# Kernel optimization log

Hardware: AMD Instinct MI355X
Metric: run time of the kernel (lower is better)

The kernel has to match this reference:

```python
import jax, jax.numpy as jnp
import numpy as np

N = 50000   # nodes
E = 800000  # edges (avg degree 16)
D = 256     # hidden_dims
V = 3       # num_views
C = 10      # num_classes


def setup_inputs() -> dict:
    key = jax.random.key(0)
    ks = jax.random.split(key, 24)
    def nrm(k, shp, scale):
        return jax.random.normal(k, shp, dtype=jnp.float32) * jnp.float32(scale)
    dims = [1000, 800, 600]
    inp = {}
    for i, d in enumerate(dims):
        inp[f"x{i}"] = nrm(ks[i], (N, d), 1.0)
        inp[f"p{i}w1"] = nrm(ks[3 + 2 * i], (d, D), 1.0 / np.sqrt(d))
        inp[f"p{i}w2"] = nrm(ks[4 + 2 * i], (D, D), 1.0 / np.sqrt(D))
    inp["edge_row"] = jax.random.randint(ks[10], (E,), 0, N)
    inp["edge_col"] = jax.random.randint(ks[11], (E,), 0, N)
    inp["edge_val"] = jax.random.uniform(ks[12], (E,), dtype=jnp.float32) / 16.0  # ~normalized adj values
    inp["vw1"] = nrm(ks[13], (V, 1), 1.0)
    inp["vw2"] = nrm(ks[14], (1, V), 1.0)
    inp["fw1"] = nrm(ks[15], (D, 16), 1.0 / np.sqrt(D))
    inp["fw2"] = nrm(ks[16], (16, D), 0.25)
    inp["m1"] = nrm(ks[17], (D + V, D // 2), 1.0 / np.sqrt(D + V))
    inp["m2"] = nrm(ks[18], (D // 2, D + V), 1.0 / np.sqrt(D // 2))
    inp["g0"] = nrm(ks[19], (D + V, D + V), 1.0 / np.sqrt(D + V))
    inp["g1"] = nrm(ks[20], (D + V, D + V), 1.0 / np.sqrt(D + V))
    inp["g2"] = nrm(ks[21], (D + V, C), 1.0 / np.sqrt(D + V))
    return inp


def _spmm(row, col, val, x):
    # torch.spmm(adj, x) with adj given as COO edge list
    return jax.ops.segment_sum(val[:, None] * x[col], row, num_segments=N)


def reference(x0, x1, x2, p0w1, p0w2, p1w1, p1w2, p2w1, p2w2,
              edge_row, edge_col, edge_val,
              vw1, vw2, fw1, fw2, m1, m2, g0, g1, g2):
    # per-view projection MLPs (bias-free, dropout off in eval)
    h0 = jax.nn.relu(x0 @ p0w1) @ p0w2
    h1 = jax.nn.relu(x1 @ p1w1) @ p1w2
    h2 = jax.nn.relu(x2 @ p2w1) @ p2w2
    h = jnp.stack([h0, h1, h2], axis=2)  # [N, D, V]

    pool_view = h.mean(axis=1)  # [N, V]
    pool_feat = h.mean(axis=2)  # [N, D]
    view_x = jax.nn.sigmoid(jax.nn.relu(pool_view @ vw1) @ vw2)  # [N, V]
    feat_x = jax.nn.sigmoid(jax.nn.relu(pool_feat @ fw1) @ fw2)  # [N, D]

    vf = jax.nn.relu(jnp.concatenate([view_x, feat_x], axis=1) @ m1) @ m2  # [N, V+D]
    view_w = jax.nn.sigmoid(vf[:, :V])[:, None, :]  # [N, 1, V]
    feat_w = jax.nn.sigmoid(vf[:, V:])[:, :, None]  # [N, D, 1]

    out1 = h * view_w
    out2 = h * feat_w
    # fus_type == 'self': [N, V] ++ [N, D] -> [N, D+V]
    z = jnp.concatenate([out1.mean(axis=1), out2.mean(axis=2)], axis=1)

    # 3-layer GCN: spmm -> linear -> tanh (tanh also on last layer per default activation)
    for g in (g0, g1, g2):
        z = jnp.tanh(_spmm(edge_row, edge_col, edge_val, z) @ g)
    return z
```

## Files before the change

### kernel.cpp

```cpp
#include <hip/hip_runtime.h>
#include <hip/hip_bf16.h>
#include <cmath>
#include <cstdint>

using bf16 = __bf16;
typedef __bf16 bf16x8 __attribute__((ext_vector_type(8)));
typedef __bf16 bf16x4 __attribute__((ext_vector_type(4)));
typedef float f32x4 __attribute__((ext_vector_type(4)));

#define DEVI __device__ __forceinline__

DEVI int pcidx(int m, int c) { return (m << 2) + (c ^ ((m >> 1) & 3)); }

DEVI void gload16(const void* g, void* l) {
  __builtin_amdgcn_global_load_lds(
      (const __attribute__((address_space(1))) void*)g,
      (__attribute__((address_space(3))) void*)l, 16, 0, 0);
}

template <int ACT, bool AF32>
__global__ __launch_bounds__(256) void gemm_k(
    const void* __restrict__ Ap, const bf16* __restrict__ Bt,
    void* __restrict__ Cp, int Mreal, int K, int ldA, int Ncols, int ldC,
    float scale, int NT, const float* __restrict__ pfx,
    const float* __restrict__ pvx) {
  __shared__ __align__(16) bf16 lA[128 * 32];
  __shared__ __align__(16) bf16 lB[128 * 32];
  const int tid = threadIdx.x;
  const int nwg = gridDim.x;
  const int q8 = nwg >> 3, r8 = nwg & 7;
  const int xcd = blockIdx.x & 7, idx = blockIdx.x >> 3;
  const int wgid =
      (xcd < r8 ? xcd * (q8 + 1) : r8 * (q8 + 1) + (xcd - r8) * q8) + idx;
  const int m0 = (wgid / NT) * 128, n0 = (wgid % NT) * 128;

  const int w = tid >> 6, lane = tid & 63;
  const int wm = w >> 1, wn = w & 1;
  const int lm = lane & 15, lg = lane >> 4;

  f32x4 acc[4][4] = {};

  const int nkt = K / 32;
  for (int kt = 0; kt < nkt; ++kt) {
    const int k0 = kt * 32;
#pragma unroll
    for (int i = 0; i < 2; i++) {
      int q = i * 256 + tid;
      int row = q >> 2, slot = q & 3;
      int c = slot ^ ((row >> 1) & 3);
      const bf16* src = Bt + (size_t)(n0 + row) * K + k0 + c * 8;
      bf16* dst = lB + (size_t)(i * 256 + (tid & 192)) * 8;
      gload16(src, dst);
    }
    if constexpr (AF32) {
      const float* Af = (const float*)Ap;
      int row = tid >> 1, h = tid & 1;
      int gm = m0 + row;
      int kb = k0 + h * 16;
      const float* Ar = Af + (size_t)gm * ldA;
      bf16x8 v0, v1;
      if (gm < Mreal && kb + 16 <= ldA) {
        f32x4 f0 = *(const f32x4*)(Ar + kb);
        f32x4 f1 = *(const f32x4*)(Ar + kb + 4);
        f32x4 f2 = *(const f32x4*)(Ar + kb + 8);
        f32x4 f3 = *(const f32x4*)(Ar + kb + 12);
#pragma unroll
        for (int j = 0; j < 4; j++) {
          v0[j] = (bf16)f0[j];
          v0[4 + j] = (bf16)f1[j];
          v1[j] = (bf16)f2[j];
          v1[4 + j] = (bf16)f3[j];
        }
      } else {
#pragma unroll
        for (int j = 0; j < 8; j++) {
          v0[j] = (bf16)((gm < Mreal && kb + j < ldA) ? Ar[kb + j] : 0.f);
          v1[j] = (bf16)((gm < Mreal && kb + 8 + j < ldA) ? Ar[kb + 8 + j] : 0.f);
        }
      }
      *(bf16x8*)&lA[(size_t)pcidx(row, h * 2) * 8] = v0;
      *(bf16x8*)&lA[(size_t)pcidx(row, h * 2 + 1) * 8] = v1;
    } else {
      const bf16* Ab = (const bf16*)Ap;
#pragma unroll
      for (int i = 0; i < 2; i++) {
        int q = i * 256 + tid;
        int row = q >> 2, slot = q & 3;
        int c = slot ^ ((row >> 1) & 3);
        const bf16* src = Ab + (size_t)(m0 + row) * K + k0 + c * 8;
        bf16* dst = lA + (size_t)(i * 256 + (tid & 192)) * 8;
        gload16(src, dst);
      }
    }
    asm volatile("s_waitcnt vmcnt(0)" ::: "memory");
    __syncthreads();
    bf16x8 af[4], bfr[4];
#pragma unroll
    for (int mi = 0; mi < 4; ++mi) {
      int m = wm * 64 + mi * 16 + lm;
      af[mi] = *(const bf16x8*)&lA[(size_t)pcidx(m, lg) * 8];
    }
#pragma unroll
    for (int ni = 0; ni < 4; ++ni) {
      int n = wn * 64 + ni * 16 + lm;
      bfr[ni] = *(const bf16x8*)&lB[(size_t)pcidx(n, lg) * 8];
    }
#pragma unroll
    for (int mi = 0; mi < 4; ++mi)
#pragma unroll
      for (int ni = 0; ni < 4; ++ni)
        acc[mi][ni] = __builtin_amdgcn_mfma_f32_16x16x32_bf16(
            af[mi], bfr[ni], acc[mi][ni], 0, 0, 0);
    __syncthreads();
  }
#pragma unroll
  for (int mi = 0; mi < 4; ++mi) {
#pragma unroll
    for (int ni = 0; ni < 4; ++ni) {
#pragma unroll
      for (int r = 0; r < 4; ++r) {
        int row = m0 + wm * 64 + mi * 16 + lg * 4 + r;
        int col = n0 + wn * 64 + ni * 16 + lm;
        if (row < Mreal && col < Ncols) {
          float x = acc[mi][ni][r] * scale;
          if constexpr (ACT == 0)
            ((float*)Cp)[(size_t)row * ldC + col] = x;
          else if constexpr (ACT == 1)
            ((bf16*)Cp)[(size_t)row * ldC + col] = (bf16)fmaxf(x, 0.f);
          else if constexpr (ACT == 3)
            ((bf16*)Cp)[(size_t)row * ldC + col] = (bf16)tanhf(x);
          else if constexpr (ACT == 4)
            ((float*)Cp)[(size_t)row * ldC + col] = tanhf(x);
          else if constexpr (ACT == 5) {
            float sig = 1.f / (1.f + __expf(-x));
            float mul;
            if (col >= 32) mul = pfx[(size_t)row * 256 + (col - 32)];
            else if (col < 3) mul = pvx[(size_t)row * 4 + col];
            else mul = 0.f;
            ((bf16*)Cp)[(size_t)row * ldC + col] = (bf16)(sig * mul);
          }
        }
      }
    }
  }
}

struct WJob {
  const float* src;
  bf16* dst;
  int Np, W, K, Nsrc, sN, Kp, cofs, kch, blkEnd;
};
struct WJobs { WJob j[14]; };

__global__ void wcvt_k(WJobs J) {
  int b = blockIdx.x;
  int ji = 0;
  while (b >= J.j[ji].blkEnd) ji++;
  const WJob job = J.j[ji];
  int lb = b - (ji ? J.j[ji - 1].blkEnd : 0);
  int n = lb / job.kch, bk = lb % job.kch;
  int k = bk * 256 + (int)threadIdx.x;
  if (k >= job.W) return;
  float v = 0.f;
  if (k < job.K && n < job.Nsrc) v = job.src[(size_t)k * job.sN + n];
  job.dst[(size_t)n * job.Kp + job.cofs + k] = (bf16)v;
}

__global__ void w2rs_k(const float* w0, const float* w1, const float* w2,
                       float* out) {
  int v = blockIdx.x, k = threadIdx.x;
  const float* w = v == 0 ? w0 : (v == 1 ? w1 : w2);
  float s = 0.f;
  for (int d = 0; d < 256; d++) s += w[(size_t)k * 256 + d];
  out[v * 256 + k] = s;
}

__global__ __launch_bounds__(256) void gate_k(
    const bf16* __restrict__ t, const float* __restrict__ pf,
    const float* __restrict__ w2rs, const float* __restrict__ vw1,
    const float* __restrict__ vw2, const float* __restrict__ fw1,
    const float* __restrict__ fw2, bf16* __restrict__ c,
    float* __restrict__ pv, int N) {
  __shared__ __align__(16) float pfs[4][260];
  __shared__ __align__(16) float usm[4][16];
  const int wid = threadIdx.x >> 6, lane = threadIdx.x & 63;
  const int n = blockIdx.x * 4 + wid;
  if (n >= N) return;
  const int g = lane >> 4, j = lane & 15;

  f32x4 pfv = *(const f32x4*)(pf + (size_t)n * 256 + lane * 4);
  *(f32x4*)&pfs[wid][lane * 4] = pfv;

  size_t tb = (size_t)n * 768;
  bf16x4 t0 = *(const bf16x4*)(t + tb + lane * 4);
  bf16x4 t1 = *(const bf16x4*)(t + tb + 256 + lane * 4);
  bf16x4 t2 = *(const bf16x4*)(t + tb + 512 + lane * 4);
  f32x4 wr0 = *(const f32x4*)(w2rs + lane * 4);
  f32x4 wr1 = *(const f32x4*)(w2rs + 256 + lane * 4);
  f32x4 wr2 = *(const f32x4*)(w2rs + 512 + lane * 4);
  float s0 = 0.f, s1 = 0.f, s2 = 0.f;
#pragma unroll
  for (int cc = 0; cc < 4; cc++) {
    s0 += (float)t0[cc] * wr0[cc];
    s1 += (float)t1[cc] * wr1[cc];
    s2 += (float)t2[cc] * wr2[cc];
  }
#pragma unroll
  for (int o = 32; o > 0; o >>= 1) {
    s0 += __shfl_xor(s0, o);
    s1 += __shfl_xor(s1, o);
    s2 += __shfl_xor(s2, o);
  }
  const float p0 = s0 * (1.f / 256.f), p1 = s1 * (1.f / 256.f),
              p2 = s2 * (1.f / 256.f);
  const float av = fmaxf(p0 * vw1[0] + p1 * vw1[1] + p2 * vw1[2], 0.f);
  const float vx0 = 1.f / (1.f + __expf(-av * vw2[0]));
  const float vx1 = 1.f / (1.f + __expf(-av * vw2[1]));
  const float vx2 = 1.f / (1.f + __expf(-av * vw2[2]));

  __builtin_amdgcn_wave_barrier();
  float uj = 0.f;
#pragma unroll
  for (int kk = 0; kk < 64; kk++) {
    int k = g * 64 + ((kk + g * 8) & 63);
    uj += pfs[wid][k] * fw1[k * 16 + j];
  }
  uj += __shfl_xor(uj, 16);
  uj += __shfl_xor(uj, 32);
  uj = fmaxf(uj, 0.f);
  if (lane < 16) usm[wid][lane] = uj;
  __builtin_amdgcn_wave_barrier();

  float ur[16];
  *(f32x4*)&ur[0] = *(const f32x4*)&usm[wid][0];
  *(f32x4*)&ur[4] = *(const f32x4*)&usm[wid][4];
  *(f32x4*)&ur[8] = *(const f32x4*)&usm[wid][8];
  *(f32x4*)&ur[12] = *(const f32x4*)&usm[wid][12];
  f32x4 fx = {0.f, 0.f, 0.f, 0.f};
#pragma unroll
  for (int jj = 0; jj < 16; jj++) {
    f32x4 wv = *(const f32x4*)(fw2 + (size_t)jj * 256 + lane * 4);
#pragma unroll
    for (int cc = 0; cc < 4; cc++) fx[cc] += ur[jj] * wv[cc];
  }
  size_t cb = (size_t)n * 288;
  bf16x4 outv;
#pragma unroll
  for (int cc = 0; cc < 4; cc++)
    outv[cc] = (bf16)(1.f / (1.f + __expf(-fx[cc])));
  *(bf16x4*)(c + cb + 32 + lane * 4) = outv;
  if (lane < 8) {
    bf16x4 hv;
#pragma unroll
    for (int cc = 0; cc < 4; cc++) {
      int pos = lane * 4 + cc;
      float vv = pos == 0 ? vx0 : (pos == 1 ? vx1 : (pos == 2 ? vx2 : 0.f));
      hv[cc] = (bf16)vv;
    }
    *(bf16x4*)(c + cb + lane * 4) = hv;
  }
  if (lane < 3) pv[(size_t)n * 4 + lane] = lane == 0 ? p0 : (lane == 1 ? p1 : p2);
}

__global__ void zero_k(int* p, int n) {
  int i = blockIdx.x * 256 + threadIdx.x;
  if (i < n) p[i] = 0;
}
__global__ void hist_k(const int* __restrict__ row, int* __restrict__ cnt, int E) {
  int e = blockIdx.x * 256 + threadIdx.x;
  if (e < E) atomicAdd(&cnt[row[e]], 1);
}
__global__ void s1_k(const int* cnt, int* bsum, int n) {
  __shared__ int sh[256];
  int i = blockIdx.x * 256 + threadIdx.x;
  sh[threadIdx.x] = (i < n) ? cnt[i] : 0;
  __syncthreads();
  for (int o = 128; o > 0; o >>= 1) {
    if ((int)threadIdx.x < o) sh[threadIdx.x] += sh[threadIdx.x + o];
    __syncthreads();
  }
  if (threadIdx.x == 0) bsum[blockIdx.x] = sh[0];
}
__global__ void s2_k(const int* bsum, int* bofs, int nb) {
  __shared__ int sh[256];
  int t = threadIdx.x;
  int v = (t < nb) ? bsum[t] : 0;
  sh[t] = v;
  __syncthreads();
  for (int o = 1; o < 256; o <<= 1) {
    int add = (t >= o) ? sh[t - o] : 0;
    __syncthreads();
    sh[t] += add;
    __syncthreads();
  }
  if (t < nb) bofs[t] = sh[t] - v;
}
__global__ void s3_k(const int* cnt, const int* bofs, int* starts, int* cursor,
                     int n, int total) {
  __shared__ int sh[256];
  int t = threadIdx.x, i = blockIdx.x * 256 + t;
  int v = (i < n) ? cnt[i] : 0;
  sh[t] = v;
  __syncthreads();
  for (int o = 1; o < 256; o <<= 1) {
    int add = (t >= o) ? sh[t - o] : 0;
    __syncthreads();
    sh[t] += add;
    __syncthreads();
  }
  if (i < n) {
    int ex = bofs[blockIdx.x] + sh[t] - v;
    starts[i] = ex;
    cursor[i] = ex;
  }
  if (i == 0) starts[n] = total;
}
__global__ void scat_k(const int* __restrict__ row, const int* __restrict__ col,
                       const float* __restrict__ val, int* __restrict__ cursor,
                       int* __restrict__ ccol, float* __restrict__ cval, int E) {
  int e = blockIdx.x * 256 + threadIdx.x;
  if (e < E) {
    int r = row[e];
    int p = atomicAdd(&cursor[r], 1);
    ccol[p] = col[e];
    cval[p] = val[e];
  }
}

__global__ __launch_bounds__(256) void spmm_k(
    const int* __restrict__ starts, const int* __restrict__ ccol,
    const float* __restrict__ cval, const bf16* __restrict__ z,
    bf16* __restrict__ s) {
  int r = blockIdx.x, t = threadIdx.x;
  int e0 = starts[r], e1 = starts[r + 1];
  float a0 = 0.f, a1 = 0.f;
  int e = e0;
  for (; e + 4 <= e1; e += 4) {
    int c0 = ccol[e], c1 = ccol[e + 1], c2 = ccol[e + 2], c3 = ccol[e + 3];
    float v0 = cval[e], v1 = cval[e + 1], v2 = cval[e + 2], v3 = cval[e + 3];
    const bf16* z0 = z + (size_t)c0 * 288;
    const bf16* z1 = z + (size_t)c1 * 288;
    const bf16* z2 = z + (size_t)c2 * 288;
    const bf16* z3 = z + (size_t)c3 * 288;
    float b0 = (float)z0[t], b1 = (float)z1[t], b2 = (float)z2[t],
          b3 = (float)z3[t];
    a0 += v0 * b0 + v1 * b1 + v2 * b2 + v3 * b3;
    if (t < 32) {
      a1 += v0 * (float)z0[256 + t] + v1 * (float)z1[256 + t] +
            v2 * (float)z2[256 + t] + v3 * (float)z3[256 + t];
    }
  }
  for (; e < e1; e++) {
    int cc = ccol[e];
    float v = cval[e];
    const bf16* zp = z + (size_t)cc * 288;
    a0 += v * (float)zp[t];
    if (t < 32) a1 += v * (float)zp[256 + t];
  }
  size_t sb = (size_t)r * 288;
  s[sb + t] = (bf16)a0;
  if (t < 32) s[sb + 256 + t] = (bf16)a1;
}

extern "C" void kernel_launch(void* const* d_in, const int* in_sizes, int n_in,
                              void* d_out, int out_size, void* d_ws,
                              size_t ws_size, hipStream_t stream) {
  const float* x0 = (const float*)d_in[0];
  const float* p0w1 = (const float*)d_in[1];
  const float* p0w2 = (const float*)d_in[2];
  const float* x1 = (const float*)d_in[3];
  const float* p1w1 = (const float*)d_in[4];
  const float* p1w2 = (const float*)d_in[5];
  const float* x2 = (const float*)d_in[6];
  const float* p2w1 = (const float*)d_in[7];
  const float* p2w2 = (const float*)d_in[8];
  const int* erow = (const int*)d_in[9];
  const int* ecol = (const int*)d_in[10];
  const float* evalp = (const float*)d_in[11];
  const float* vw1 = (const float*)d_in[12];
  const float* vw2 = (const float*)d_in[13];
  const float* fw1 = (const float*)d_in[14];
  const float* fw2 = (const float*)d_in[15];
  const float* m1 = (const float*)d_in[16];
  const float* m2 = (const float*)d_in[17];
  const float* g0 = (const float*)d_in[18];
  const float* g1 = (const float*)d_in[19];
  const float* g2 = (const float*)d_in[20];

  const int N = 50000;
  const int MP = 50048;
  const int NB = 391;
  const int E = in_sizes[9];

  char* p = (char*)d_ws;
  auto alloc = [&](size_t bytes) -> char* {
    char* r = p;
    p += (bytes + 255) & ~(size_t)255;
    return r;
  };
  bf16* t = (bf16*)alloc((size_t)MP * 768 * 2);
  bf16* w1T0 = (bf16*)alloc((size_t)256 * 1024 * 2);
  bf16* w1T1 = (bf16*)alloc((size_t)256 * 832 * 2);
  bf16* w1T2 = (bf16*)alloc((size_t)256 * 640 * 2);
  bf16* W2sT = (bf16*)alloc((size_t)256 * 768 * 2);
  float* w2rs = (float*)alloc(768 * 4);
  bf16* m1T = (bf16*)alloc((size_t)128 * 288 * 2);
  bf16* m2T = (bf16*)alloc((size_t)384 * 128 * 2);
  bf16* g0T = (bf16*)alloc((size_t)384 * 288 * 2);
  bf16* g1T = (bf16*)alloc((size_t)384 * 288 * 2);
  bf16* g2T = (bf16*)alloc((size_t)128 * 288 * 2);
  float* pf = (float*)alloc((size_t)N * 256 * 4);
  float* pv = (float*)alloc((size_t)N * 4 * 4);
  bf16* c = (bf16*)alloc((size_t)MP * 288 * 2);
  int* cnt = (int*)alloc((size_t)50004 * 4);
  int* starts = (int*)alloc((size_t)50004 * 4);
  int* cursor = (int*)alloc((size_t)50004 * 4);
  int* bsum = (int*)alloc(1024);
  int* bofs = (int*)alloc(1024);
  int* ccol = (int*)alloc((size_t)E * 4);
  float* cval = (float*)alloc((size_t)E * 4);
  bf16* u = t;
  bf16* z = t + (size_t)MP * 416;
  bf16* s = c;
  if ((size_t)(p - (char*)d_ws) > ws_size) return;

  WJobs J;
  auto setj = [&](int idx, const float* src, bf16* dst, int Np, int W, int K,
                  int Nsrc, int sN, int Kp, int cofs) {
    WJob& jj = J.j[idx];
    jj.src = src; jj.dst = dst; jj.Np = Np; jj.W = W; jj.K = K; jj.Nsrc = Nsrc;
    jj.sN = sN; jj.Kp = Kp; jj.cofs = cofs; jj.kch = (W + 255) / 256;
    jj.blkEnd = 0;
  };
  setj(0, p0w1, w1T0, 256, 1024, 1000, 256, 256, 1024, 0);
  setj(1, p1w1, w1T1, 256, 832, 800, 256, 256, 832, 0);
  setj(2, p2w1, w1T2, 256, 640, 600, 256, 256, 640, 0);
  setj(3, p0w2, W2sT, 256, 256, 256, 256, 256, 768, 0);
  setj(4, p1w2, W2sT, 256, 256, 256, 256, 256, 768, 256);
  setj(5, p2w2, W2sT, 256, 256, 256, 256, 256, 768, 512);
  setj(6, m1, m1T, 128, 32, 3, 128, 128, 288, 0);
  setj(7, m1 + 3 * 128, m1T, 128, 256, 256, 128, 128, 288, 32);
  setj(8, m2, m2T, 32, 128, 128, 3, 259, 128, 0);
  setj(9, m2 + 3, m2T + (size_t)32 * 128, 256, 128, 128, 256, 259, 128, 0);
  setj(10, g0, g0T, 384, 32, 3, 259, 259, 288, 0);
  setj(11, g0 + 3 * 259, g0T, 384, 256, 256, 259, 259, 288, 32);
  setj(12, g1, g1T, 384, 288, 259, 259, 259, 288, 0);
  setj(13, g2, g2T, 128, 288, 259, 10, 10, 288, 0);
  int cum = 0;
  for (int i = 0; i < 14; i++) {
    cum += J.j[i].Np * J.j[i].kch;
    J.j[i].blkEnd = cum;
  }
  wcvt_k<<<cum, 256, 0, stream>>>(J);
  w2rs_k<<<3, 256, 0, stream>>>(p0w2, p1w2, p2w2, w2rs);

  gemm_k<1, true><<<NB * 2, 256, 0, stream>>>(x0, w1T0, t, N, 1024, 1000, 256, 768, 1.f, 2, nullptr, nullptr);
  gemm_k<1, true><<<NB * 2, 256, 0, stream>>>(x1, w1T1, t + 256, N, 832, 800, 256, 768, 1.f, 2, nullptr, nullptr);
  gemm_k<1, true><<<NB * 2, 256, 0, stream>>>(x2, w1T2, t + 512, N, 640, 600, 256, 768, 1.f, 2, nullptr, nullptr);
  gemm_k<0, false><<<NB * 2, 256, 0, stream>>>(t, W2sT, pf, N, 768, 768, 256, 256, 1.f / 3.f, 2, nullptr, nullptr);
  gate_k<<<(N + 3) / 4, 256, 0, stream>>>(t, pf, w2rs, vw1, vw2, fw1, fw2, c, pv, N);
  gemm_k<1, false><<<NB * 1, 256, 0, stream>>>(c, m1T, u, N, 288, 288, 128, 128, 1.f, 1, nullptr, nullptr);
  gemm_k<5, false><<<NB * 3, 256, 0, stream>>>(u, m2T, z, N, 128, 128, 288, 288, 1.f, 3, pf, pv);

  zero_k<<<196, 256, 0, stream>>>(cnt, N);
  hist_k<<<(E + 255) / 256, 256, 0, stream>>>(erow, cnt, E);
  s1_k<<<196, 256, 0, stream>>>(cnt, bsum, N);
  s2_k<<<1, 256, 0, stream>>>(bsum, bofs, 196);
  s3_k<<<196, 256, 0, stream>>>(cnt, bofs, starts, cursor, N, E);
  scat_k<<<(E + 255) / 256, 256, 0, stream>>>(erow, ecol, evalp, cursor, ccol, cval, E);

  spmm_k<<<N, 256, 0, stream>>>(starts, ccol, cval, z, s);
  gemm_k<3, false><<<NB * 3, 256, 0, stream>>>(s, g0T, z, N, 288, 288, 288, 288, 1.f, 3, nullptr, nullptr);
  spmm_k<<<N, 256, 0, stream>>>(starts, ccol, cval, z, s);
  gemm_k<3, false><<<NB * 3, 256, 0, stream>>>(s, g1T, z, N, 288, 288, 288, 288, 1.f, 3, nullptr, nullptr);
  spmm_k<<<N, 256, 0, stream>>>(starts, ccol, cval, z, s);
  gemm_k<4, false><<<NB * 1, 256, 0, stream>>>(s, g2T, d_out, N, 288, 288, 10, 10, 1.f, 1, nullptr, nullptr);
}
```

Baseline: 1.278 ms.

## Double-buffer GEMM LDS tiles and merge three view projection GEMMs into one launch

Gives the bf16 GEMM two LDS buffers so the next K-tile's global-to-LDS loads are issued before the MFMAs on the current tile, and drops the per-iteration trailing barrier. Adds a separate gemm3_k that runs all three fp32-input first-layer projections in a single launch through a job table. That kernel prefetches the next fp32 A tile into registers during compute and converts it to bf16 afterwards. The intent is to hide memory latency behind MFMA work and cut launch and tail overhead, at the cost of twice the LDS per block and more registers, which may lower occupancy.

```diff
diff --git a/kernel.cpp b/kernel.cpp
--- a/kernel.cpp
+++ b/kernel.cpp
@@ -18,20 +18,21 @@
       (__attribute__((address_space(3))) void*)l, 16, 0, 0);
 }
 
-template <int ACT, bool AF32>
+DEVI int xcd_swz(int lb, int nwg) {
+  int q8 = nwg >> 3, r8 = nwg & 7;
+  int xcd = lb & 7, idx = lb >> 3;
+  return (xcd < r8 ? xcd * (q8 + 1) : r8 * (q8 + 1) + (xcd - r8) * q8) + idx;
+}
+
+template <int ACT>
 __global__ __launch_bounds__(256) void gemm_k(
-    const void* __restrict__ Ap, const bf16* __restrict__ Bt,
-    void* __restrict__ Cp, int Mreal, int K, int ldA, int Ncols, int ldC,
-    float scale, int NT, const float* __restrict__ pfx,
-    const float* __restrict__ pvx) {
-  __shared__ __align__(16) bf16 lA[128 * 32];
-  __shared__ __align__(16) bf16 lB[128 * 32];
+    const bf16* __restrict__ Ab, const bf16* __restrict__ Bt,
+    void* __restrict__ Cp, int Mreal, int K, int Ncols, int ldC, float scale,
+    int NT, const float* __restrict__ pfx, const float* __restrict__ pvx) {
+  __shared__ __align__(16) bf16 lA[2][128 * 32];
+  __shared__ __align__(16) bf16 lB[2][128 * 32];
   const int tid = threadIdx.x;
-  const int nwg = gridDim.x;
-  const int q8 = nwg >> 3, r8 = nwg & 7;
-  const int xcd = blockIdx.x & 7, idx = blockIdx.x >> 3;
-  const int wgid =
-      (xcd < r8 ? xcd * (q8 + 1) : r8 * (q8 + 1) + (xcd - r8) * q8) + idx;
+  const int wgid = xcd_swz(blockIdx.x, gridDim.x);
   const int m0 = (wgid / NT) * 128, n0 = (wgid % NT) * 128;
 
   const int w = tid >> 6, lane = tid & 63;
@@ -40,70 +41,41 @@
 
   f32x4 acc[4][4] = {};
 
-  const int nkt = K / 32;
-  for (int kt = 0; kt < nkt; ++kt) {
-    const int k0 = kt * 32;
+  auto issueAB = [&](int buf, int k0) {
 #pragma unroll
     for (int i = 0; i < 2; i++) {
       int q = i * 256 + tid;
       int row = q >> 2, slot = q & 3;
       int c = slot ^ ((row >> 1) & 3);
-      const bf16* src = Bt + (size_t)(n0 + row) * K + k0 + c * 8;
-      bf16* dst = lB + (size_t)(i * 256 + (tid & 192)) * 8;
-      gload16(src, dst);
-    }
-    if constexpr (AF32) {
-      const float* Af = (const float*)Ap;
-      int row = tid >> 1, h = tid & 1;
-      int gm = m0 + row;
-      int kb = k0 + h * 16;
-      const float* Ar = Af + (size_t)gm * ldA;
-      bf16x8 v0, v1;
-      if (gm < Mreal && kb + 16 <= ldA) {
-        f32x4 f0 = *(const f32x4*)(Ar + kb);
-        f32x4 f1 = *(const f32x4*)(Ar + kb + 4);
-        f32x4 f2 = *(const f32x4*)(Ar + kb + 8);
-        f32x4 f3 = *(const f32x4*)(Ar + kb + 12);
-#pragma unroll
-        for (int j = 0; j < 4; j++) {
-          v0[j] = (bf16)f0[j];
-          v0[4 + j] = (bf16)f1[j];
-          v1[j] = (bf16)f2[j];
-          v1[4 + j] = (bf16)f3[j];
-        }
-      } else {
-#pragma unroll
-        for (int j = 0; j < 8; j++) {
-          v0[j] = (bf16)((gm < Mreal && kb + j < ldA) ? Ar[kb + j] : 0.f);
-          v1[j] = (bf16)((gm < Mreal && kb + 8 + j < ldA) ? Ar[kb + 8 + j] : 0.f);
-        }
-      }
-      *(bf16x8*)&lA[(size_t)pcidx(row, h * 2) * 8] = v0;
-      *(bf16x8*)&lA[(size_t)pcidx(row, h * 2 + 1) * 8] = v1;
-    } else {
-      const bf16* Ab = (const bf16*)Ap;
-#pragma unroll
-      for (int i = 0; i < 2; i++) {
-        int q = i * 256 + tid;
-        int row = q >> 2, slot = q & 3;
-        int c = slot ^ ((row >> 1) & 3);
-        const bf16* src = Ab + (size_t)(m0 + row) * K + k0 + c * 8;
-        bf16* dst = lA + (size_t)(i * 256 + (tid & 192)) * 8;
-        gload16(src, dst);
-      }
-    }
-    asm volatile("s_waitcnt vmcnt(0)" ::: "memory");
-    __syncthreads();
+      gload16(Bt + (size_t)(n0 + row) * K + k0 + c * 8,
+              &lB[buf][(size_t)(i * 256 + (tid & 192)) * 8]);
+    }
+#pragma unroll
+    for (int i = 0; i < 2; i++) {
+      int q = i * 256 + tid;
+      int row = q >> 2, slot = q & 3;
+      int c = slot ^ ((row >> 1) & 3);
+      gload16(Ab + (size_t)(m0 + row) * K + k0 + c * 8,
+              &lA[buf][(size_t)(i * 256 + (tid & 192)) * 8]);
+    }
+  };
+
+  const int nkt = K / 32;
+  issueAB(0, 0);
+  __syncthreads();
+  for (int kt = 0; kt < nkt; ++kt) {
+    const int cur = kt & 1, nxt = cur ^ 1;
+    if (kt + 1 < nkt) issueAB(nxt, (kt + 1) * 32);
     bf16x8 af[4], bfr[4];
 #pragma unroll
     for (int mi = 0; mi < 4; ++mi) {
       int m = wm * 64 + mi * 16 + lm;
-      af[mi] = *(const bf16x8*)&lA[(size_t)pcidx(m, lg) * 8];
+      af[mi] = *(const bf16x8*)&lA[cur][(size_t)pcidx(m, lg) * 8];
     }
 #pragma unroll
     for (int ni = 0; ni < 4; ++ni) {
       int n = wn * 64 + ni * 16 + lm;
-      bfr[ni] = *(const bf16x8*)&lB[(size_t)pcidx(n, lg) * 8];
+      bfr[ni] = *(const bf16x8*)&lB[cur][(size_t)pcidx(n, lg) * 8];
     }
 #pragma unroll
     for (int mi = 0; mi < 4; ++mi)
@@ -111,7 +83,7 @@
       for (int ni = 0; ni < 4; ++ni)
         acc[mi][ni] = __builtin_amdgcn_mfma_f32_16x16x32_bf16(
             af[mi], bfr[ni], acc[mi][ni], 0, 0, 0);
-    __syncthreads();
+    if (kt + 1 < nkt) __syncthreads();
   }
 #pragma unroll
   for (int mi = 0; mi < 4; ++mi) {
@@ -140,6 +112,117 @@
             ((bf16*)Cp)[(size_t)row * ldC + col] = (bf16)(sig * mul);
           }
         }
+      }
+    }
+  }
+}
+
+struct GJob { const float* A; const bf16* Bt; bf16* C; int K, ldA, blkEnd; };
+struct GJobs { GJob j[3]; };
+
+__global__ __launch_bounds__(256) void gemm3_k(GJobs G, int Mreal) {
+  __shared__ __align__(16) bf16 lA[2][128 * 32];
+  __shared__ __align__(16) bf16 lB[2][128 * 32];
+  const int tid = threadIdx.x;
+  int ji = 0;
+  while ((int)blockIdx.x >= G.j[ji].blkEnd) ji++;
+  const GJob job = G.j[ji];
+  const int jstart = ji ? G.j[ji - 1].blkEnd : 0;
+  const int wgid = xcd_swz(blockIdx.x - jstart, job.blkEnd - jstart);
+  const int m0 = (wgid >> 1) * 128, n0 = (wgid & 1) * 128;
+  const int K = job.K, ldA = job.ldA;
+
+  const int w = tid >> 6, lane = tid & 63;
+  const int wm = w >> 1, wn = w & 1;
+  const int lm = lane & 15, lg = lane >> 4;
+
+  const int arow = tid >> 1, h = tid & 1;
+  const int gm = m0 + arow;
+  const float* Ar = job.A + (size_t)gm * ldA;
+
+  f32x4 f[4];
+  auto issueA = [&](int k0) {
+    int kb = k0 + h * 16;
+    if (gm < Mreal && kb + 16 <= ldA) {
+      f[0] = *(const f32x4*)(Ar + kb);
+      f[1] = *(const f32x4*)(Ar + kb + 4);
+      f[2] = *(const f32x4*)(Ar + kb + 8);
+      f[3] = *(const f32x4*)(Ar + kb + 12);
+    } else {
+#pragma unroll
+      for (int q = 0; q < 4; q++)
+#pragma unroll
+        for (int j = 0; j < 4; j++)
+          f[q][j] = (gm < Mreal && kb + q * 4 + j < ldA) ? Ar[kb + q * 4 + j] : 0.f;
+    }
+  };
+  auto writeA = [&](int buf) {
+    bf16x8 v0, v1;
+#pragma unroll
+    for (int j = 0; j < 4; j++) {
+      v0[j] = (bf16)f[0][j];
+      v0[4 + j] = (bf16)f[1][j];
+      v1[j] = (bf16)f[2][j];
+      v1[4 + j] = (bf16)f[3][j];
+    }
+    *(bf16x8*)&lA[buf][(size_t)pcidx(arow, h * 2) * 8] = v0;
+    *(bf16x8*)&lA[buf][(size_t)pcidx(arow, h * 2 + 1) * 8] = v1;
+  };
+  auto issueB = [&](int buf, int k0) {
+#pragma unroll
+    for (int i = 0; i < 2; i++) {
+      int q = i * 256 + tid;
+      int row = q >> 2, slot = q & 3;
+      int c = slot ^ ((row >> 1) & 3);
+      gload16(job.Bt + (size_t)(n0 + row) * K + k0 + c * 8,
+              &lB[buf][(size_t)(i * 256 + (tid & 192)) * 8]);
+    }
+  };
+
+  f32x4 acc[4][4] = {};
+  const int nkt = K / 32;
+  issueB(0, 0);
+  issueA(0);
+  writeA(0);
+  __syncthreads();
+  for (int kt = 0; kt < nkt; ++kt) {
+    const int cur = kt & 1, nxt = cur ^ 1;
+    if (kt + 1 < nkt) {
+      issueB(nxt, (kt + 1) * 32);
+      issueA((kt + 1) * 32);
+    }
+    bf16x8 af[4], bfr[4];
+#pragma unroll
+    for (int mi = 0; mi < 4; ++mi) {
+      int m = wm * 64 + mi * 16 + lm;
+      af[mi] = *(const bf16x8*)&lA[cur][(size_t)pcidx(m, lg) * 8];
+    }
+#pragma unroll
+    for (int ni = 0; ni < 4; ++ni) {
+      int n = wn * 64 + ni * 16 + lm;
+      bfr[ni] = *(const bf16x8*)&lB[cur][(size_t)pcidx(n, lg) * 8];
+    }
+#pragma unroll
+    for (int mi = 0; mi < 4; ++mi)
+#pragma unroll
+      for (int ni = 0; ni < 4; ++ni)
+        acc[mi][ni] = __builtin_amdgcn_mfma_f32_16x16x32_bf16(
+            af[mi], bfr[ni], acc[mi][ni], 0, 0, 0);
+    if (kt + 1 < nkt) {
+      writeA(nxt);
+      __syncthreads();
+    }
+  }
+#pragma unroll
+  for (int mi = 0; mi < 4; ++mi) {
+#pragma unroll
+    for (int ni = 0; ni < 4; ++ni) {
+#pragma unroll
+      for (int r = 0; r < 4; ++r) {
+        int row = m0 + wm * 64 + mi * 16 + lg * 4 + r;
+        int col = n0 + wn * 64 + ni * 16 + lm;
+        if (row < Mreal && col < 256)
+          job.C[(size_t)row * 768 + col] = (bf16)fmaxf(acc[mi][ni][r], 0.f);
       }
     }
   }
@@ -454,13 +537,15 @@
   wcvt_k<<<cum, 256, 0, stream>>>(J);
   w2rs_k<<<3, 256, 0, stream>>>(p0w2, p1w2, p2w2, w2rs);
 
-  gemm_k<1, true><<<NB * 2, 256, 0, stream>>>(x0, w1T0, t, N, 1024, 1000, 256, 768, 1.f, 2, nullptr, nullptr);
-  gemm_k<1, true><<<NB * 2, 256, 0, stream>>>(x1, w1T1, t + 256, N, 832, 800, 256, 768, 1.f, 2, nullptr, nullptr);
-  gemm_k<1, true><<<NB * 2, 256, 0, stream>>>(x2, w1T2, t + 512, N, 640, 600, 256, 768, 1.f, 2, nullptr, nullptr);
-  gemm_k<0, false><<<NB * 2, 256, 0, stream>>>(t, W2sT, pf, N, 768, 768, 256, 256, 1.f / 3.f, 2, nullptr, nullptr);
+  GJobs G;
+  G.j[0] = {x0, w1T0, t, 1024, 1000, NB * 2};
+  G.j[1] = {x1, w1T1, t + 256, 832, 800, NB * 4};
+  G.j[2] = {x2, w1T2, t + 512, 640, 600, NB * 6};
+  gemm3_k<<<NB * 6, 256, 0, stream>>>(G, N);
+  gemm_k<0><<<NB * 2, 256, 0, stream>>>(t, W2sT, pf, N, 768, 256, 256, 1.f / 3.f, 2, nullptr, nullptr);
   gate_k<<<(N + 3) / 4, 256, 0, stream>>>(t, pf, w2rs, vw1, vw2, fw1, fw2, c, pv, N);
-  gemm_k<1, false><<<NB * 1, 256, 0, stream>>>(c, m1T, u, N, 288, 288, 128, 128, 1.f, 1, nullptr, nullptr);
-  gemm_k<5, false><<<NB * 3, 256, 0, stream>>>(u, m2T, z, N, 128, 128, 288, 288, 1.f, 3, pf, pv);
+  gemm_k<1><<<NB * 1, 256, 0, stream>>>(c, m1T, u, N, 288, 128, 128, 1.f, 1, nullptr, nullptr);
+  gemm_k<5><<<NB * 3, 256, 0, stream>>>(u, m2T, z, N, 128, 288, 288, 1.f, 3, pf, pv);
 
   zero_k<<<196, 256, 0, stream>>>(cnt, N);
   hist_k<<<(E + 255) / 256, 256, 0, stream>>>(erow, cnt, E);
@@ -470,9 +555,9 @@
   scat_k<<<(E + 255) / 256, 256, 0, stream>>>(erow, ecol, evalp, cursor, ccol, cval, E);
 
   spmm_k<<<N, 256, 0, stream>>>(starts, ccol, cval, z, s);
-  gemm_k<3, false><<<NB * 3, 256, 0, stream>>>(s, g0T, z, N, 288, 288, 288, 288, 1.f, 3, nullptr, nullptr);
+  gemm_k<3><<<NB * 3, 256, 0, stream>>>(s, g0T, z, N, 288, 288, 288, 1.f, 3, nullptr, nullptr);
   spmm_k<<<N, 256, 0, stream>>>(starts, ccol, cval, z, s);
-  gemm_k<3, false><<<NB * 3, 256, 0, stream>>>(s, g1T, z, N, 288, 288, 288, 288, 1.f, 3, nullptr, nullptr);
+  gemm_k<3><<<NB * 3, 256, 0, stream>>>(s, g1T, z, N, 288, 288, 288, 1.f, 3, nullptr, nullptr);
   spmm_k<<<N, 256, 0, stream>>>(starts, ccol, cval, z, s);
-  gemm_k<4, false><<<NB * 1, 256, 0, stream>>>(s, g2T, d_out, N, 288, 288, 10, 10, 1.f, 1, nullptr, nullptr);
-}
+  gemm_k<4><<<NB * 1, 256, 0, stream>>>(s, g2T, d_out, N, 288, 10, 10, 1.f, 1, nullptr, nullptr);
+}
```

Result: faster. 1.235 ms (-3.4%).
